# Optimization experiments

Measured on AMD Instinct MI355X. Metric: run time of the kernel, lower is better.

The kernel has to match this reference:

```python
import jax, jax.numpy as jnp
import numpy as np

WINDOW = 128
LOOK_BACKWARD = 1
LOOK_FORWARD = 0
DIM_HEAD = 64
ROPE_BASE = 10000.0


def look_around(x, backward=LOOK_BACKWARD, forward=LOOK_FORWARD, pad_value=-1):
    # x: [b, w, n, ...] -> pad window axis, gather shifted windows, concat along n axis
    w = x.shape[1]
    pads = [(0, 0)] * x.ndim
    pads[1] = (backward, forward)
    padded = jnp.pad(x, pads, constant_values=pad_value)
    return jnp.concatenate([padded[:, i:i + w] for i in range(backward + forward + 1)], axis=2)


def _rotate_half(x):
    x1, x2 = jnp.split(x, 2, axis=-1)
    return jnp.concatenate([-x2, x1], axis=-1)


def apply_rotary(bq, bk):
    # sinusoidal embeddings computed over the look-around key length j; queries use the last n positions
    j = bk.shape[2]
    n = bq.shape[2]
    inv_freq = 1.0 / (ROPE_BASE ** (jnp.arange(0, DIM_HEAD, 2, dtype=jnp.float32) / DIM_HEAD))
    t = jnp.arange(j, dtype=jnp.float32)
    freqs = t[:, None] * inv_freq[None, :]          # [j, d/2]
    freqs = jnp.concatenate([freqs, freqs], axis=-1)  # [j, d]
    q_freqs = freqs[-n:]
    bq = bq * jnp.cos(q_freqs) + _rotate_half(bq) * jnp.sin(q_freqs)
    bk = bk * jnp.cos(freqs) + _rotate_half(bk) * jnp.sin(freqs)
    return bq, bk


def setup_inputs() -> dict:
    key = jax.random.key(0)
    kq, kk, kv = jax.random.split(key, 3)
    shape = (4, 8, 4096, 64)
    return {
        'q': jax.random.normal(kq, shape, dtype=jnp.float32),
        'k': jax.random.normal(kk, shape, dtype=jnp.float32),
        'v': jax.random.normal(kv, shape, dtype=jnp.float32),
    }


def reference(q, k, v):
    B, H, N, D = q.shape
    b = B * H
    q_ = q.reshape(b, N, D)
    k_ = k.reshape(b, N, D)
    v_ = v.reshape(b, N, D)
    w = N // WINDOW
    scale = D ** -0.5

    seq = jnp.arange(N)
    b_t = seq.reshape(1, w, WINDOW)                           # [1, w, n]

    bq = q_.reshape(b, w, WINDOW, D) * scale
    bk = look_around(k_.reshape(b, w, WINDOW, D), pad_value=-1.0)  # [b, w, j, d]
    bv = look_around(v_.reshape(b, w, WINDOW, D), pad_value=-1.0)

    bq, bk = apply_rotary(bq, bk)

    bq_t = b_t[..., :, None]                                  # [1, w, n, 1]
    bq_k = look_around(b_t, pad_value=-1)[..., None, :]        # [1, w, 1, j]
    pad_mask = bq_k == -1
    causal_mask = bq_t < bq_k

    sim = jnp.einsum('bwie,bwje->bwij', bq, bk)                # [b, w, n, j]
    mask_value = -jnp.finfo(sim.dtype).max
    sim = jnp.where(causal_mask | pad_mask, mask_value, sim)

    attn = jax.nn.softmax(sim, axis=-1)
    out = jnp.einsum('bwij,bwje->bwie', attn, bv)
    return out.reshape(B, H, N, D)
```

## Files before the change

### kernel.cpp

```cpp
#include <hip/hip_runtime.h>
#include <float.h>

typedef __attribute__((ext_vector_type(8))) _Float16 f16x8;
typedef __attribute__((ext_vector_type(4))) _Float16 f16x4;
typedef __attribute__((ext_vector_type(4))) float f32x4;

#define WIN 128
#define SEQ 4096
#define DH 64
#define KSTR 72
#define VSTR 264
#define PSTR 136
#define VOFF 36864
#define L2B_OVER 0.41524101186092156f

__launch_bounds__(512, 4)
__global__ void lattn_kernel(const float* __restrict__ q,
                             const float* __restrict__ k,
                             const float* __restrict__ v,
                             float* __restrict__ out) {
  __shared__ __align__(16) char smem[70656];
  _Float16* ksm = (_Float16*)smem;
  _Float16* psm = (_Float16*)smem;
  _Float16* vsm = (_Float16*)(smem + VOFF);

  const int bid  = blockIdx.x;
  const int lbid = (bid & 7) * 128 + (bid >> 3);
  const int bh   = lbid >> 5;
  const int win  = lbid & 31;
  const int tid  = threadIdx.x;
  const int wv   = tid >> 6;
  const int lane = tid & 63;
  const int c    = lane & 15;
  const int g    = lane >> 4;

  const int qrow = 16 * wv + c;
  const float* qp = q + ((size_t)bh * SEQ + (size_t)win * WIN + qrow) * DH;
  const float4 x0 = *(const float4*)(qp + 8 * g);
  const float4 x1 = *(const float4*)(qp + 8 * g + 4);
  const float4 y0 = *(const float4*)(qp + 8 * g + 32);
  const float4 y1 = *(const float4*)(qp + 8 * g + 36);

  #pragma unroll
  for (int it = 0; it < 4; ++it) {
    int hi  = it * 8 + wv;
    int row = c + 16 * (hi >> 1);
    int p   = g + 4 * (hi & 1);
    long grow = (long)win * WIN - WIN + row;
    float4 lo = {0.f, 0.f, 0.f, 0.f}, hi4 = {0.f, 0.f, 0.f, 0.f};
    if (grow >= 0) {
      const float4* src = (const float4*)(k + ((size_t)bh * SEQ + grow) * DH);
      lo  = src[p];
      hi4 = src[p + 8];
    }
    float pos = (float)row;
    f16x4 rl, rh;
    #pragma unroll
    for (int j = 0; j < 4; ++j) {
      float sn, cs;
      __sincosf(pos * exp2f(-(float)(4 * p + j) * L2B_OVER), &sn, &cs);
      float x = ((const float*)&lo)[j];
      float y = ((const float*)&hi4)[j];
      rl[j] = (_Float16)(x * cs - y * sn);
      rh[j] = (_Float16)(y * cs + x * sn);
    }
    *(f16x4*)(&ksm[row * KSTR + 4 * p])      = rl;
    *(f16x4*)(&ksm[row * KSTR + 4 * p + 32]) = rh;
  }

  #pragma unroll
  for (int it = 0; it < 8; ++it) {
    int hi  = it * 8 + wv;
    int row = c + 16 * (hi & 15);
    int pf  = g + 4 * (hi >> 4);
    long grow = (long)win * WIN - WIN + row;
    float4 val = {0.f, 0.f, 0.f, 0.f};
    if (grow >= 0)
      val = *(const float4*)(v + ((size_t)bh * SEQ + grow) * DH + 4 * pf);
    #pragma unroll
    for (int i = 0; i < 4; ++i)
      vsm[(4 * pf + i) * VSTR + row] = (_Float16)(((const float*)&val)[i]);
  }

  f16x8 qf0, qf1;
  {
    float pos = (float)(128 + qrow);
    #pragma unroll
    for (int j = 0; j < 4; ++j) {
      float sn, cs;
      __sincosf(pos * exp2f(-(float)(8 * g + j) * L2B_OVER), &sn, &cs);
      float xa = ((const float*)&x0)[j], ya = ((const float*)&y0)[j];
      qf0[j]     = (_Float16)((xa * cs - ya * sn) * 0.125f);
      qf1[j]     = (_Float16)((ya * cs + xa * sn) * 0.125f);
      __sincosf(pos * exp2f(-(float)(8 * g + 4 + j) * L2B_OVER), &sn, &cs);
      float xb = ((const float*)&x1)[j], yb = ((const float*)&y1)[j];
      qf0[4 + j] = (_Float16)((xb * cs - yb * sn) * 0.125f);
      qf1[4 + j] = (_Float16)((yb * cs + xb * sn) * 0.125f);
    }
  }

  __syncthreads();

  f32x4 acc[16];
  #pragma unroll
  for (int mt = 0; mt < 16; ++mt) acc[mt] = (f32x4){0.f, 0.f, 0.f, 0.f};

  #pragma unroll
  for (int mt = 0; mt < 16; ++mt) {
    f16x8 kf0 = *(const f16x8*)(&ksm[(16 * mt + c) * KSTR + 8 * g]);
    f16x8 kf1 = *(const f16x8*)(&ksm[(16 * mt + c) * KSTR + 32 + 8 * g]);
    acc[mt] = __builtin_amdgcn_mfma_f32_16x16x32_f16(kf0, qf0, acc[mt], 0, 0, 0);
    acc[mt] = __builtin_amdgcn_mfma_f32_16x16x32_f16(kf1, qf1, acc[mt], 0, 0, 0);
  }

  const int qi   = qrow;
  const int kmin = (win == 0) ? 128 : 0;
  float m = -FLT_MAX;
  #pragma unroll
  for (int mt = 0; mt < 16; ++mt) {
    #pragma unroll
    for (int r = 0; r < 4; ++r) {
      int j = 16 * mt + 4 * g + r;
      bool ok = (j <= qi + 128) && (j >= kmin);
      float s = ok ? acc[mt][r] : -FLT_MAX;
      acc[mt][r] = s;
      m = fmaxf(m, s);
    }
  }
  m = fmaxf(m, __shfl_xor(m, 16));
  m = fmaxf(m, __shfl_xor(m, 32));

  float sm = 0.f;
  #pragma unroll
  for (int mt = 0; mt < 16; ++mt) {
    #pragma unroll
    for (int r = 0; r < 4; ++r) {
      float p = __expf(acc[mt][r] - m);
      acc[mt][r] = p;
      sm += p;
    }
  }
  sm += __shfl_xor(sm, 16);
  sm += __shfl_xor(sm, 32);
  const float rinv = 1.0f / sm;

  __syncthreads();

  f32x4 oacc[4];
  #pragma unroll
  for (int nt = 0; nt < 4; ++nt) oacc[nt] = (f32x4){0.f, 0.f, 0.f, 0.f};

  _Float16* pw = psm + wv * 16 * PSTR;

  #pragma unroll
  for (int h = 0; h < 2; ++h) {
    if (h) {
      asm volatile("s_waitcnt lgkmcnt(0)" ::: "memory");
      __builtin_amdgcn_sched_barrier(0);
    }
    #pragma unroll
    for (int mt8 = 0; mt8 < 8; ++mt8) {
      int mt = 8 * h + mt8;
      f16x4 pv4;
      #pragma unroll
      for (int r = 0; r < 4; ++r) pv4[r] = (_Float16)(acc[mt][r] * rinv);
      *(f16x4*)(&pw[c * PSTR + 16 * mt8 + 4 * g]) = pv4;
    }
    asm volatile("s_waitcnt lgkmcnt(0)" ::: "memory");
    __builtin_amdgcn_sched_barrier(0);

    #pragma unroll
    for (int ks = 0; ks < 4; ++ks) {
      f16x8 pf = *(const f16x8*)(&pw[c * PSTR + 32 * ks + 8 * g]);
      #pragma unroll
      for (int nt = 0; nt < 4; ++nt) {
        f16x8 vf = *(const f16x8*)(&vsm[(16 * nt + c) * VSTR + 128 * h + 32 * ks + 8 * g]);
        oacc[nt] = __builtin_amdgcn_mfma_f32_16x16x32_f16(pf, vf, oacc[nt], 0, 0, 0);
      }
    }
  }

  float* ob = out + ((size_t)bh * SEQ + (size_t)win * WIN + 16 * wv) * DH;
  #pragma unroll
  for (int nt = 0; nt < 4; ++nt) {
    #pragma unroll
    for (int r = 0; r < 4; ++r) {
      ob[(4 * g + r) * DH + 16 * nt + c] = oacc[nt][r];
    }
  }
}

extern "C" void kernel_launch(void* const* d_in, const int* in_sizes, int n_in,
                              void* d_out, int out_size, void* d_ws, size_t ws_size,
                              hipStream_t stream) {
  const float* q = (const float*)d_in[0];
  const float* k = (const float*)d_in[1];
  const float* v = (const float*)d_in[2];
  float* out = (float*)d_out;
  dim3 grid(32 * 32);
  lattn_kernel<<<grid, 512, 0, stream>>>(q, k, v, out);
}
```

Measured before the change: 43.34 us.

## Give P its own LDS region, transpose V via register 4x4 blocks, drop sync

P staging gets a dedicated small per-wave LDS region instead of aliasing the K buffer, which removes the second __syncthreads. P is now written and consumed in 32-key chunks, one k-step at a time. The V load now reads 4 rows per thread and transposes them in registers, so each thread does vectorized f16x4 LDS stores instead of scalar ones. Boundary handling clamps the row index instead of branching, so the first window loads real data that the mask discards. Q loads move after the K/V staging. Total LDS grows slightly, which may affect occupancy, and the finer-grained P chunks add more waitcnt barriers.

```diff
diff --git a/kernel.cpp b/kernel.cpp
--- a/kernel.cpp
+++ b/kernel.cpp
@@ -9,9 +9,10 @@
 #define SEQ 4096
 #define DH 64
 #define KSTR 72
-#define VSTR 264
-#define PSTR 136
+#define VSTR 260
+#define PC 40
 #define VOFF 36864
+#define POFF (VOFF + DH * VSTR * 2)
 #define L2B_OVER 0.41524101186092156f
 
 __launch_bounds__(512, 4)
@@ -19,10 +20,10 @@
                              const float* __restrict__ k,
                              const float* __restrict__ v,
                              float* __restrict__ out) {
-  __shared__ __align__(16) char smem[70656];
+  __shared__ __align__(16) char smem[POFF + 8 * 16 * PC * 2];
   _Float16* ksm = (_Float16*)smem;
-  _Float16* psm = (_Float16*)smem;
   _Float16* vsm = (_Float16*)(smem + VOFF);
+  _Float16* psm = (_Float16*)(smem + POFF);
 
   const int bid  = blockIdx.x;
   const int lbid = (bid & 7) * 128 + (bid >> 3);
@@ -34,25 +35,19 @@
   const int c    = lane & 15;
   const int g    = lane >> 4;
 
-  const int qrow = 16 * wv + c;
-  const float* qp = q + ((size_t)bh * SEQ + (size_t)win * WIN + qrow) * DH;
-  const float4 x0 = *(const float4*)(qp + 8 * g);
-  const float4 x1 = *(const float4*)(qp + 8 * g + 4);
-  const float4 y0 = *(const float4*)(qp + 8 * g + 32);
-  const float4 y1 = *(const float4*)(qp + 8 * g + 36);
+  const long kbase = (long)win * WIN - WIN;
+  const float* kb = k + (size_t)bh * SEQ * DH;
+  const float* vb = v + (size_t)bh * SEQ * DH;
 
   #pragma unroll
   for (int it = 0; it < 4; ++it) {
     int hi  = it * 8 + wv;
     int row = c + 16 * (hi >> 1);
     int p   = g + 4 * (hi & 1);
-    long grow = (long)win * WIN - WIN + row;
-    float4 lo = {0.f, 0.f, 0.f, 0.f}, hi4 = {0.f, 0.f, 0.f, 0.f};
-    if (grow >= 0) {
-      const float4* src = (const float4*)(k + ((size_t)bh * SEQ + grow) * DH);
-      lo  = src[p];
-      hi4 = src[p + 8];
-    }
+    long grow = kbase + row; grow = grow < 0 ? 0 : grow;
+    const float4* src = (const float4*)(kb + grow * DH);
+    float4 lo  = src[p];
+    float4 hi4 = src[p + 8];
     float pos = (float)row;
     f16x4 rl, rh;
     #pragma unroll
@@ -69,19 +64,30 @@
   }
 
   #pragma unroll
-  for (int it = 0; it < 8; ++it) {
-    int hi  = it * 8 + wv;
-    int row = c + 16 * (hi & 15);
-    int pf  = g + 4 * (hi >> 4);
-    long grow = (long)win * WIN - WIN + row;
-    float4 val = {0.f, 0.f, 0.f, 0.f};
-    if (grow >= 0)
-      val = *(const float4*)(v + ((size_t)bh * SEQ + grow) * DH + 4 * pf);
-    #pragma unroll
-    for (int i = 0; i < 4; ++i)
-      vsm[(4 * pf + i) * VSTR + row] = (_Float16)(((const float*)&val)[i]);
-  }
-
+  for (int it = 0; it < 2; ++it) {
+    int kq = g + 4 * (it * 8 + wv);
+    int dq = c;
+    float4 r[4];
+    #pragma unroll
+    for (int i = 0; i < 4; ++i) {
+      long grow = kbase + 4 * kq + i; grow = grow < 0 ? 0 : grow;
+      r[i] = *(const float4*)(vb + grow * DH + 4 * dq);
+    }
+    #pragma unroll
+    for (int j = 0; j < 4; ++j) {
+      f16x4 w;
+      #pragma unroll
+      for (int i = 0; i < 4; ++i) w[i] = (_Float16)(((const float*)&r[i])[j]);
+      *(f16x4*)(&vsm[(4 * dq + j) * VSTR + 4 * kq]) = w;
+    }
+  }
+
+  const int qrow = 16 * wv + c;
+  const float* qp = q + ((size_t)bh * SEQ + (size_t)win * WIN + qrow) * DH;
+  const float4 x0 = *(const float4*)(qp + 8 * g);
+  const float4 x1 = *(const float4*)(qp + 8 * g + 4);
+  const float4 y0 = *(const float4*)(qp + 8 * g + 32);
+  const float4 y1 = *(const float4*)(qp + 8 * g + 36);
   f16x8 qf0, qf1;
   {
     float pos = (float)(128 + qrow);
@@ -144,39 +150,34 @@
   sm += __shfl_xor(sm, 32);
   const float rinv = 1.0f / sm;
 
-  __syncthreads();
-
   f32x4 oacc[4];
   #pragma unroll
   for (int nt = 0; nt < 4; ++nt) oacc[nt] = (f32x4){0.f, 0.f, 0.f, 0.f};
 
-  _Float16* pw = psm + wv * 16 * PSTR;
-
-  #pragma unroll
-  for (int h = 0; h < 2; ++h) {
-    if (h) {
+  _Float16* pw = psm + wv * 16 * PC;
+
+  #pragma unroll
+  for (int ks = 0; ks < 8; ++ks) {
+    if (ks) {
       asm volatile("s_waitcnt lgkmcnt(0)" ::: "memory");
       __builtin_amdgcn_sched_barrier(0);
     }
     #pragma unroll
-    for (int mt8 = 0; mt8 < 8; ++mt8) {
-      int mt = 8 * h + mt8;
+    for (int t = 0; t < 2; ++t) {
+      int mt = 2 * ks + t;
       f16x4 pv4;
       #pragma unroll
       for (int r = 0; r < 4; ++r) pv4[r] = (_Float16)(acc[mt][r] * rinv);
-      *(f16x4*)(&pw[c * PSTR + 16 * mt8 + 4 * g]) = pv4;
+      *(f16x4*)(&pw[c * PC + 16 * t + 4 * g]) = pv4;
     }
     asm volatile("s_waitcnt lgkmcnt(0)" ::: "memory");
     __builtin_amdgcn_sched_barrier(0);
 
-    #pragma unroll
-    for (int ks = 0; ks < 4; ++ks) {
-      f16x8 pf = *(const f16x8*)(&pw[c * PSTR + 32 * ks + 8 * g]);
-      #pragma unroll
-      for (int nt = 0; nt < 4; ++nt) {
-        f16x8 vf = *(const f16x8*)(&vsm[(16 * nt + c) * VSTR + 128 * h + 32 * ks + 8 * g]);
-        oacc[nt] = __builtin_amdgcn_mfma_f32_16x16x32_f16(pf, vf, oacc[nt], 0, 0, 0);
-      }
+    f16x8 pf = *(const f16x8*)(&pw[c * PC + 8 * g]);
+    #pragma unroll
+    for (int nt = 0; nt < 4; ++nt) {
+      f16x8 vf = *(const f16x8*)(&vsm[(16 * nt + c) * VSTR + 32 * ks + 8 * g]);
+      oacc[nt] = __builtin_amdgcn_mfma_f32_16x16x32_f16(pf, vf, oacc[nt], 0, 0, 0);
     }
   }
 
```

Result: slower. 52.65 us (+21.5%).
